# Kernel tuning notes

Measured on AMD Instinct MI355X. Metric: run time of the kernel, lower is better.

Reference implementation:

```python
import jax, jax.numpy as jnp
import numpy as np

B, HT, WD, DIM = 8, 128, 128, 512
NUM_HEADS = 8
HEAD_DIM = DIM // NUM_HEADS
K = 7  # kernel_size
R = K // 2


def setup_inputs() -> dict:
    key = jax.random.key(0)
    k1, k2 = jax.random.split(key)
    x = jax.random.normal(k1, (B, HT, WD, DIM), dtype=jnp.float32)
    # nn.Linear(dim, 2*dim, bias=False); stored as [in, out] so y = x @ W_qk
    W_qk = jax.random.normal(k2, (DIM, 2 * DIM), dtype=jnp.float32) * (DIM ** -0.5)
    return {"x": x, "W_qk": W_qk}


def reference(x, W_qk):
    Bsz, H, W, C = x.shape
    scale = HEAD_DIM ** -0.5
    # qk projection -> [B,H,W,2,heads,head_dim]
    qk = (x @ W_qk).reshape(Bsz, H, W, 2, NUM_HEADS, HEAD_DIM)
    q = qk[..., 0, :, :] * scale          # [B,H,W,hd,d]
    kk = qk[..., 1, :, :]                 # [B,H,W,hd,d]
    # NATTEN border handling: window start clamped so the KxK window stays inside.
    starts_i = jnp.clip(jnp.arange(H) - R, 0, H - K)  # [H]
    starts_j = jnp.clip(jnp.arange(W) - R, 0, W - K)  # [W]
    attn = []
    for ki in range(K):
        k_row = kk[:, starts_i + ki]          # [B,H,W,hd,d] (gather rows)
        for kj in range(K):
            k_n = k_row[:, :, starts_j + kj]  # [B,H,W,hd,d] (gather cols)
            attn.append(jnp.einsum('bhwnd,bhwnd->bhwn', q, k_n))
    attn = jnp.stack(attn, axis=-1)           # [B,H,W,hd,K*K]
    return jnp.transpose(attn, (0, 3, 1, 2, 4))  # [B,hd,H,W,K*K]
```

## Files before the change

### kernel.cpp

```cpp
#include <hip/hip_runtime.h>

typedef __attribute__((ext_vector_type(8))) short short8;
typedef __attribute__((ext_vector_type(4))) float floatx4;

__device__ __forceinline__ unsigned short f2bf(float f) {
  union { float f; unsigned u; } x; x.f = f;
  unsigned u = x.u + 0x7fffu + ((x.u >> 16) & 1u);
  return (unsigned short)(u >> 16);
}

__device__ __forceinline__ void gload_lds16(const void* g, void* l) {
  __builtin_amdgcn_global_load_lds(
      (const __attribute__((address_space(1))) unsigned int*)g,
      (__attribute__((address_space(3))) unsigned int*)l, 16, 0, 0);
}


__global__ __launch_bounds__(256) void cvt_x(const float4* __restrict__ x,
                                             uint2* __restrict__ o) {
  size_t idx = (size_t)blockIdx.x * 256 + threadIdx.x;
  float4 v = x[idx];
  uint2 r;
  r.x = (unsigned)f2bf(v.x) | ((unsigned)f2bf(v.y) << 16);
  r.y = (unsigned)f2bf(v.z) | ((unsigned)f2bf(v.w) << 16);
  o[idx] = r;
}

__global__ __launch_bounds__(256) void cvt_w(const float* __restrict__ w,
                                             unsigned short* __restrict__ wt) {
  int tid = blockIdx.x * 256 + threadIdx.x;
  int n = tid >> 9, k = tid & 511;
  float v = w[k * 1024 + n];
  if (n < 512) v *= 0.125f;
  wt[tid] = f2bf(v);
}

__global__ __launch_bounds__(512, 2) void gemm_bt(const unsigned short* __restrict__ A,
                                                  const unsigned short* __restrict__ Bt,
                                                  unsigned short* __restrict__ C) {
  __shared__ __align__(16) unsigned short lds_a[2][8 * 256 * 8];
  __shared__ __align__(16) unsigned short lds_b[2][8 * 256 * 8];

  const int t = threadIdx.x;
  const int bid = blockIdx.x;
  const int wg = (bid & 7) * 256 + (bid >> 3);
  const int mtile = wg >> 2;
  const int ntile = wg & 3;
  const int m0 = mtile * 256, n0 = ntile * 256;
  const int wave = t >> 6, lane = t & 63;
  const int wm = (wave >> 2) * 128, wn = (wave & 3) * 64;
  const int kg = lane >> 4, rr = lane & 15;

  const unsigned short* aptr[4];
  const unsigned short* bptr[4];
#pragma unroll
  for (int p = 0; p < 4; ++p) {
    int S = t + p * 512, kgrp = S >> 8, row = S & 255;
    aptr[p] = &A[(size_t)(m0 + row) * 512 + kgrp * 8];
    bptr[p] = &Bt[(size_t)(n0 + row) * 512 + kgrp * 8];
  }

#pragma unroll
  for (int p = 0; p < 4; ++p) {
    gload_lds16(aptr[p], &lds_a[0][(t + p * 512) * 8]);
    gload_lds16(bptr[p], &lds_b[0][(t + p * 512) * 8]);
  }
  __syncthreads();

  floatx4 acc[8][4] = {};
  int cur = 0;
#pragma unroll 1
  for (int step = 0; step < 8; ++step) {
    if (step < 7) {
      int k0n = (step + 1) * 64;
#pragma unroll
      for (int p = 0; p < 4; ++p) {
        gload_lds16(aptr[p] + k0n, &lds_a[cur ^ 1][(t + p * 512) * 8]);
        gload_lds16(bptr[p] + k0n, &lds_b[cur ^ 1][(t + p * 512) * 8]);
      }
    }

#pragma unroll
    for (int kc = 0; kc < 2; ++kc) {
      const int kbase = (kc * 4 + kg) * 256;
      short8 af[8], bf[4];
#pragma unroll
      for (int i = 0; i < 8; ++i)
        af[i] = *(const short8*)&lds_a[cur][(kbase + wm + i * 16 + rr) * 8];
#pragma unroll
      for (int j = 0; j < 4; ++j)
        bf[j] = *(const short8*)&lds_b[cur][(kbase + wn + j * 16 + rr) * 8];
#pragma unroll
      for (int i = 0; i < 8; ++i)
#pragma unroll
        for (int j = 0; j < 4; ++j)
          acc[i][j] = __builtin_amdgcn_mfma_f32_16x16x32_bf16(af[i], bf[j], acc[i][j], 0, 0, 0);
    }

    __syncthreads();
    cur ^= 1;
  }

#pragma unroll
  for (int i = 0; i < 8; ++i) {
    int mrow = m0 + wm + i * 16 + (lane >> 4) * 4;
#pragma unroll
    for (int j = 0; j < 4; ++j) {
      int ncol = n0 + wn + j * 16 + rr;
#pragma unroll
      for (int r = 0; r < 4; ++r)
        C[(size_t)(mrow + r) * 1024 + ncol] = f2bf(acc[i][j][r]);
    }
  }
}

__global__ __launch_bounds__(256) void attn_mfma(const unsigned short* __restrict__ QK,
                                                 float* __restrict__ out) {
  __shared__ __align__(16) unsigned short q_lds[128 * 64];
  __shared__ __align__(16) unsigned short k_lds[2][128 * 64];
  __shared__ __align__(16) float s_scr[4][24 * 20];
  __shared__ __align__(16) float out_lds[128 * 49];

  const int t = threadIdx.x;
  const int bid = blockIdx.x;
  const int wg = (bid & 7) * 1024 + (bid >> 3);
  const int i = wg & 127;
  const int h = (wg >> 7) & 7;
  const int b = wg >> 10;
  const int wave = t >> 6, lane = t & 63;
  const int kg = lane >> 4, rr = lane & 15;
  const int ri = min(max(i - 3, 0), 121);

  const unsigned short* qbase = QK + ((size_t)(b * 128 + i) * 128) * 1024 + h * 64;
#pragma unroll
  for (int s = 0; s < 4; ++s) {
    int S = t + s * 256;
    int j = S >> 3, pg = S & 7, lg = pg ^ (j & 7);
    gload_lds16(qbase + (size_t)j * 1024 + lg * 8, &q_lds[S * 8]);
  }
  {
    const unsigned short* kb = QK + ((size_t)(b * 128 + ri) * 128) * 1024 + 512 + h * 64;
#pragma unroll
    for (int s = 0; s < 4; ++s) {
      int S = t + s * 256;
      int c = S >> 3, pg = S & 7, lg = pg ^ (c & 7);
      gload_lds16(kb + (size_t)c * 1024 + lg * 8, &k_lds[0][S * 8]);
    }
  }
  __syncthreads();

  short8 af[2][2];
#pragma unroll
  for (int jt2 = 0; jt2 < 2; ++jt2) {
    int row = (wave * 2 + jt2) * 16 + rr;
#pragma unroll
    for (int ks = 0; ks < 2; ++ks) {
      int lg = ks * 4 + kg;
      af[jt2][ks] = *(const short8*)&q_lds[(row * 8 + (lg ^ (row & 7))) * 8];
    }
  }

  const int m = lane >> 2, kj0 = lane & 3;

  for (int ki = 0; ki < 7; ++ki) {
    const int cur = ki & 1;
    if (ki < 6) {
      const unsigned short* kb =
          QK + ((size_t)(b * 128 + ri + ki + 1) * 128) * 1024 + 512 + h * 64;
#pragma unroll
      for (int s = 0; s < 4; ++s) {
        int S = t + s * 256;
        int c = S >> 3, pg = S & 7, lg = pg ^ (c & 7);
        gload_lds16(kb + (size_t)c * 1024 + lg * 8, &k_lds[cur ^ 1][S * 8]);
      }
    }
    const unsigned short* kbuf = k_lds[cur];
    float* scr = s_scr[wave];

#pragma unroll
    for (int jt2 = 0; jt2 < 2; ++jt2) {
      const int j0 = (wave * 2 + jt2) * 16;
      const int cb = min(max(j0 - 3, 0), 121);
      const int c0 = min(cb + rr, 127);
      const int c1 = min(cb + 16 + rr, 127);
      floatx4 acc0 = {0.f, 0.f, 0.f, 0.f}, acc1 = {0.f, 0.f, 0.f, 0.f};
#pragma unroll
      for (int ks = 0; ks < 2; ++ks) {
        int lg = ks * 4 + kg;
        short8 b0 = *(const short8*)&kbuf[(c0 * 8 + (lg ^ (c0 & 7))) * 8];
        short8 b1 = *(const short8*)&kbuf[(c1 * 8 + (lg ^ (c1 & 7))) * 8];
        acc0 = __builtin_amdgcn_mfma_f32_16x16x32_bf16(af[jt2][ks], b0, acc0, 0, 0, 0);
        acc1 = __builtin_amdgcn_mfma_f32_16x16x32_bf16(af[jt2][ks], b1, acc1, 0, 0, 0);
      }
      {
        int crow = (lane >> 4) * 4;
        *(floatx4*)&scr[rr * 20 + crow] = acc0;
        if (rr < 8) *(floatx4*)&scr[(16 + rr) * 20 + crow] = acc1;
      }
      asm volatile("s_waitcnt lgkmcnt(0)" ::: "memory");
      {
        int relc = min(max(j0 + m - 3, 0), 121) - cb;
        int p = j0 + m;
        out_lds[p * 49 + ki * 7 + kj0] = scr[(relc + kj0) * 20 + m];
        if (kj0 < 3)
          out_lds[p * 49 + ki * 7 + 4 + kj0] = scr[(relc + 4 + kj0) * 20 + m];
      }
      asm volatile("s_waitcnt lgkmcnt(0)" ::: "memory");
    }
    __syncthreads();
  }

  const uint4* src = (const uint4*)out_lds;
  uint4* dst = (uint4*)(out + ((size_t)(b * 8 + h) * 16384 + (size_t)i * 128) * 49);
  for (int s = t; s < 1568; s += 256) dst[s] = src[s];
}

extern "C" void kernel_launch(void* const* d_in, const int* in_sizes, int n_in,
                              void* d_out, int out_size, void* d_ws, size_t ws_size,
                              hipStream_t stream) {
  const float* x = (const float*)d_in[0];
  const float* w = (const float*)d_in[1];
  float* out = (float*)d_out;

  unsigned short* xb = (unsigned short*)d_ws;
  unsigned short* wt = xb + 67108864;
  unsigned short* qk = wt + 524288;

  cvt_x<<<65536, 256, 0, stream>>>((const float4*)x, (uint2*)xb);
  cvt_w<<<2048, 256, 0, stream>>>(w, wt);
  gemm_bt<<<2048, 512, 0, stream>>>(xb, wt, qk);
  attn_mfma<<<8192, 256, 0, stream>>>(qk, out);
}
```

Measured before the change: 875.3 us.

## Deepen async load pipelines in GEMM and attention with vmcnt-based barriers

The GEMM now uses a 4-stage ring of 32-wide K slices with three tiles in flight, replacing the 2-stage double buffer of 64-wide slices. Each step waits with s_waitcnt vmcnt plus s_barrier, so only the oldest tile has to land instead of draining all loads. The attention kernel keeps two K rows prefetched ahead and issues the next load after the compute barrier, using partial vmcnt waits in place of full __syncthreads. This targets global-memory latency stalls at the cost of more barriers per K and correctness that depends on exact vmcnt counts matching the number of outstanding loads.

```diff
diff --git a/kernel.cpp b/kernel.cpp
--- a/kernel.cpp
+++ b/kernel.cpp
@@ -38,8 +38,8 @@
 __global__ __launch_bounds__(512, 2) void gemm_bt(const unsigned short* __restrict__ A,
                                                   const unsigned short* __restrict__ Bt,
                                                   unsigned short* __restrict__ C) {
-  __shared__ __align__(16) unsigned short lds_a[2][8 * 256 * 8];
-  __shared__ __align__(16) unsigned short lds_b[2][8 * 256 * 8];
+  __shared__ __align__(16) unsigned short lds_a[4][4 * 256 * 8];
+  __shared__ __align__(16) unsigned short lds_b[4][4 * 256 * 8];
 
   const int t = threadIdx.x;
   const int bid = blockIdx.x;
@@ -51,54 +51,58 @@
   const int wm = (wave >> 2) * 128, wn = (wave & 3) * 64;
   const int kg = lane >> 4, rr = lane & 15;
 
-  const unsigned short* aptr[4];
-  const unsigned short* bptr[4];
-#pragma unroll
-  for (int p = 0; p < 4; ++p) {
+  const unsigned short* aP[2];
+  const unsigned short* bP[2];
+#pragma unroll
+  for (int p = 0; p < 2; ++p) {
     int S = t + p * 512, kgrp = S >> 8, row = S & 255;
-    aptr[p] = &A[(size_t)(m0 + row) * 512 + kgrp * 8];
-    bptr[p] = &Bt[(size_t)(n0 + row) * 512 + kgrp * 8];
-  }
-
-#pragma unroll
-  for (int p = 0; p < 4; ++p) {
-    gload_lds16(aptr[p], &lds_a[0][(t + p * 512) * 8]);
-    gload_lds16(bptr[p], &lds_b[0][(t + p * 512) * 8]);
-  }
-  __syncthreads();
+    aP[p] = &A[(size_t)(m0 + row) * 512 + kgrp * 8];
+    bP[p] = &Bt[(size_t)(n0 + row) * 512 + kgrp * 8];
+  }
+
+#pragma unroll
+  for (int tt = 0; tt < 3; ++tt) {
+#pragma unroll
+    for (int p = 0; p < 2; ++p) {
+      gload_lds16(aP[p] + tt * 32, &lds_a[tt][(t + p * 512) * 8]);
+      gload_lds16(bP[p] + tt * 32, &lds_b[tt][(t + p * 512) * 8]);
+    }
+  }
 
   floatx4 acc[8][4] = {};
-  int cur = 0;
-#pragma unroll 1
-  for (int step = 0; step < 8; ++step) {
-    if (step < 7) {
-      int k0n = (step + 1) * 64;
-#pragma unroll
-      for (int p = 0; p < 4; ++p) {
-        gload_lds16(aptr[p] + k0n, &lds_a[cur ^ 1][(t + p * 512) * 8]);
-        gload_lds16(bptr[p] + k0n, &lds_b[cur ^ 1][(t + p * 512) * 8]);
-      }
-    }
-
-#pragma unroll
-    for (int kc = 0; kc < 2; ++kc) {
-      const int kbase = (kc * 4 + kg) * 256;
-      short8 af[8], bf[4];
-#pragma unroll
-      for (int i = 0; i < 8; ++i)
-        af[i] = *(const short8*)&lds_a[cur][(kbase + wm + i * 16 + rr) * 8];
+
+#pragma unroll
+  for (int step = 0; step < 16; ++step) {
+    if (step < 14)
+      asm volatile("s_waitcnt vmcnt(8)\n\ts_barrier" ::: "memory");
+    else if (step == 14)
+      asm volatile("s_waitcnt vmcnt(4)\n\ts_barrier" ::: "memory");
+    else
+      asm volatile("s_waitcnt vmcnt(0)\n\ts_barrier" ::: "memory");
+
+    if (step + 3 < 16) {
+      const int k0n = (step + 3) * 32;
+      const int nb = (step + 3) & 3;
+#pragma unroll
+      for (int p = 0; p < 2; ++p) {
+        gload_lds16(aP[p] + k0n, &lds_a[nb][(t + p * 512) * 8]);
+        gload_lds16(bP[p] + k0n, &lds_b[nb][(t + p * 512) * 8]);
+      }
+    }
+
+    const int cur = step & 3;
+    short8 af[8], bf[4];
+#pragma unroll
+    for (int i = 0; i < 8; ++i)
+      af[i] = *(const short8*)&lds_a[cur][(kg * 256 + wm + i * 16 + rr) * 8];
+#pragma unroll
+    for (int j = 0; j < 4; ++j)
+      bf[j] = *(const short8*)&lds_b[cur][(kg * 256 + wn + j * 16 + rr) * 8];
+#pragma unroll
+    for (int i = 0; i < 8; ++i)
 #pragma unroll
       for (int j = 0; j < 4; ++j)
-        bf[j] = *(const short8*)&lds_b[cur][(kbase + wn + j * 16 + rr) * 8];
-#pragma unroll
-      for (int i = 0; i < 8; ++i)
-#pragma unroll
-        for (int j = 0; j < 4; ++j)
-          acc[i][j] = __builtin_amdgcn_mfma_f32_16x16x32_bf16(af[i], bf[j], acc[i][j], 0, 0, 0);
-    }
-
-    __syncthreads();
-    cur ^= 1;
+        acc[i][j] = __builtin_amdgcn_mfma_f32_16x16x32_bf16(af[i], bf[j], acc[i][j], 0, 0, 0);
   }
 
 #pragma unroll
@@ -138,16 +142,18 @@
     int j = S >> 3, pg = S & 7, lg = pg ^ (j & 7);
     gload_lds16(qbase + (size_t)j * 1024 + lg * 8, &q_lds[S * 8]);
   }
-  {
-    const unsigned short* kb = QK + ((size_t)(b * 128 + ri) * 128) * 1024 + 512 + h * 64;
+#pragma unroll
+  for (int kt = 0; kt < 2; ++kt) {
+    const unsigned short* kb = QK + ((size_t)(b * 128 + ri + kt) * 128) * 1024 + 512 + h * 64;
 #pragma unroll
     for (int s = 0; s < 4; ++s) {
       int S = t + s * 256;
       int c = S >> 3, pg = S & 7, lg = pg ^ (c & 7);
-      gload_lds16(kb + (size_t)c * 1024 + lg * 8, &k_lds[0][S * 8]);
-    }
-  }
-  __syncthreads();
+      gload_lds16(kb + (size_t)c * 1024 + lg * 8, &k_lds[kt][S * 8]);
+    }
+  }
+
+  asm volatile("s_waitcnt vmcnt(8)\n\ts_barrier" ::: "memory");
 
   short8 af[2][2];
 #pragma unroll
@@ -162,19 +168,14 @@
 
   const int m = lane >> 2, kj0 = lane & 3;
 
+#pragma unroll
   for (int ki = 0; ki < 7; ++ki) {
-    const int cur = ki & 1;
-    if (ki < 6) {
-      const unsigned short* kb =
-          QK + ((size_t)(b * 128 + ri + ki + 1) * 128) * 1024 + 512 + h * 64;
-#pragma unroll
-      for (int s = 0; s < 4; ++s) {
-        int S = t + s * 256;
-        int c = S >> 3, pg = S & 7, lg = pg ^ (c & 7);
-        gload_lds16(kb + (size_t)c * 1024 + lg * 8, &k_lds[cur ^ 1][S * 8]);
-      }
-    }
-    const unsigned short* kbuf = k_lds[cur];
+    if (ki < 6)
+      asm volatile("s_waitcnt vmcnt(4)\n\ts_barrier" ::: "memory");
+    else
+      asm volatile("s_waitcnt vmcnt(0)\n\ts_barrier" ::: "memory");
+
+    const unsigned short* kbuf = k_lds[ki & 1];
     float* scr = s_scr[wave];
 
 #pragma unroll
@@ -207,7 +208,18 @@
       }
       asm volatile("s_waitcnt lgkmcnt(0)" ::: "memory");
     }
-    __syncthreads();
+
+    asm volatile("s_barrier" ::: "memory");
+    if (ki + 2 <= 6) {
+      const unsigned short* kb =
+          QK + ((size_t)(b * 128 + ri + ki + 2) * 128) * 1024 + 512 + h * 64;
+#pragma unroll
+      for (int s = 0; s < 4; ++s) {
+        int S = t + s * 256;
+        int c = S >> 3, pg = S & 7, lg = pg ^ (c & 7);
+        gload_lds16(kb + (size_t)c * 1024 + lg * 8, &k_lds[ki & 1][S * 8]);
+      }
+    }
   }
 
   const uint4* src = (const uint4*)out_lds;
```

After: 849.7 us. 2.9% less time.
